# Performance work log

Measured on AMD Instinct MI355X. Metric: run time of the kernel, lower is better.

## Reference

```python
import jax, jax.numpy as jnp
import numpy as np

NUM_NODES = 10000


def setup_inputs() -> dict:
    key = jax.random.key(0)
    k1, k2, k3, k4 = jax.random.split(key, 4)
    x = jax.random.normal(k1, (NUM_NODES, 128), dtype=jnp.float32)
    edge_index = jax.random.randint(k2, (2, 640000), 0, NUM_NODES, dtype=jnp.int64)
    W = jax.random.normal(k3, (128, 128), dtype=jnp.float32) * (1.0 / np.sqrt(128))
    b = jax.random.normal(k4, (128,), dtype=jnp.float32) * 0.01
    return {"x": x, "edge_index": edge_index, "W": W, "b": b}


def reference(x, edge_index, W, b):
    src, dst = edge_index[0], edge_index[1]
    num_nodes = x.shape[0]
    # scatter-add: aggregated[dst] += x[src]
    aggregated = jax.ops.segment_sum(x[src], dst, num_segments=num_nodes)
    # in-degree normalization (clamped at 1)
    degree = jax.ops.segment_sum(jnp.ones_like(dst, dtype=x.dtype), dst,
                                 num_segments=num_nodes)
    degree = jnp.maximum(degree, 1.0)
    aggregated = aggregated / degree[:, None]
    # linear (y = h @ W.T + b) + ReLU
    out = jax.nn.relu(jnp.einsum('nd,od->no', aggregated + x, W) + b)
    return out
```

## Files before the change

### kernel.cpp

```cpp
#include <hip/hip_runtime.h>
#include <hip/hip_bf16.h>
#include <hip/hip_fp8.h>

#define NB    64
#define EPB   10000
#define NPAD  10240
#define NPT   40
#define NGEMM 625
#define LCAP  1024

typedef __bf16 bf16_8 __attribute__((ext_vector_type(8)));
typedef float f32_2 __attribute__((ext_vector_type(2)));
typedef float f32_4 __attribute__((ext_vector_type(4)));
typedef float f32_8 __attribute__((ext_vector_type(8)));

__global__ void __launch_bounds__(256) k_fused(
    const float* __restrict__ x, const float* __restrict__ W,
    const int* __restrict__ ei, int E,
    __hip_bfloat16* __restrict__ zb, unsigned char* __restrict__ zb8,
    unsigned short* __restrict__ bins, unsigned int* __restrict__ combo) {
  __shared__ int h[NPAD / 2];
  __shared__ unsigned short sorted[EPB];
  __shared__ int wsum[4];

  if (blockIdx.x < NGEMM) {
    int rowbase = blockIdx.x * 16;
    int wid = threadIdx.x >> 6;
    int lane = threadIdx.x & 63;
    int m16 = lane & 15;
    int quad = lane >> 4;

    union { bf16_8 v; __hip_bfloat16 h8[8]; } ac[4];
    const float* arow = x + (size_t)(rowbase + m16) * 128 + quad * 8;
#pragma unroll
    for (int kk = 0; kk < 4; ++kk) {
      f32_8 af = *(const f32_8*)(arow + kk * 32);
#pragma unroll
      for (int j = 0; j < 8; ++j) ac[kk].h8[j] = __float2bfloat16(af[j]);
    }
#pragma unroll
    for (int ct = 0; ct < 2; ++ct) {
      int colbase = wid * 32 + ct * 16;
      const float* brow = W + (size_t)(colbase + m16) * 128 + quad * 8;
      f32_4 c = {0.f, 0.f, 0.f, 0.f};
#pragma unroll
      for (int kk = 0; kk < 4; ++kk) {
        f32_8 bf = *(const f32_8*)(brow + kk * 32);
        union { bf16_8 v; __hip_bfloat16 h8[8]; } bc;
#pragma unroll
        for (int j = 0; j < 8; ++j) bc.h8[j] = __float2bfloat16(bf[j]);
        c = __builtin_amdgcn_mfma_f32_16x16x32_bf16(ac[kk].v, bc.v, c, 0, 0, 0);
      }
#pragma unroll
      for (int r = 0; r < 4; ++r) {
        int row = rowbase + quad * 4 + r;
        zb[(size_t)row * 128 + colbase + m16] = __float2bfloat16(c[r]);
        zb8[(size_t)row * 128 + colbase + m16] = __hip_fp8_e4m3(c[r]).__x;
      }
    }
    return;
  }

  const int b = blockIdx.x - NGEMM;
  const int t = threadIdx.x;
  const int4* src4 = (const int4*)(ei) + b * (EPB / 4);
  const int4* dst4 = (const int4*)(ei + E) + b * (EPB / 4);

  for (int i = t; i < NPAD / 2; i += 256) h[i] = 0;
  __syncthreads();

  for (int i = t; i < EPB / 4; i += 256) {
    int4 d = dst4[i];
    atomicAdd(&h[d.x >> 1], 1 << ((d.x & 1) * 16));
    atomicAdd(&h[d.y >> 1], 1 << ((d.y & 1) * 16));
    atomicAdd(&h[d.z >> 1], 1 << ((d.z & 1) * 16));
    atomicAdd(&h[d.w >> 1], 1 << ((d.w & 1) * 16));
  }
  __syncthreads();

  int raw[NPT];
  const int lo = t * NPT;
  int sum = 0;
#pragma unroll
  for (int j = 0; j < NPT; j += 2) {
    int pair = h[(lo + j) >> 1];
    raw[j] = pair & 0xFFFF;
    raw[j + 1] = (pair >> 16) & 0xFFFF;
    sum += raw[j] + raw[j + 1];
  }
  int incl = sum;
#pragma unroll
  for (int off = 1; off < 64; off <<= 1) {
    int v = __shfl_up(incl, off);
    if ((t & 63) >= off) incl += v;
  }
  if ((t & 63) == 63) wsum[t >> 6] = incl;
  __syncthreads();
  int wb = 0;
  for (int w = 0; w < (t >> 6); ++w) wb += wsum[w];
  int run = wb + incl - sum;

  unsigned int cpack[NPT];
#pragma unroll
  for (int j = 0; j < NPT; j += 2) {
    int r0 = run; run += raw[j];
    int r1 = run; run += raw[j + 1];
    h[(lo + j) >> 1] = (r1 << 16) | r0;
    cpack[j]     = ((unsigned)raw[j] << 16) | (unsigned)r0;
    cpack[j + 1] = ((unsigned)raw[j + 1] << 16) | (unsigned)r1;
  }
  __syncthreads();

  unsigned int* crow = combo + (size_t)b * NPAD + lo;
#pragma unroll
  for (int j = 0; j < NPT; j += 4)
    *(uint4*)(crow + j) = make_uint4(cpack[j], cpack[j+1], cpack[j+2], cpack[j+3]);

  for (int i = t; i < EPB / 4; i += 256) {
    int4 s4 = src4[i];
    int4 d4 = dst4[i];
    int ss[4] = {s4.x, s4.y, s4.z, s4.w};
    int dd[4] = {d4.x, d4.y, d4.z, d4.w};
#pragma unroll
    for (int u = 0; u < 4; ++u) {
      int n = dd[u];
      int sh = (n & 1) * 16;
      int pos = (atomicAdd(&h[n >> 1], 1 << sh) >> sh) & 0xFFFF;
      sorted[pos] = (unsigned short)ss[u];
    }
  }
  __syncthreads();

  unsigned int* outb = (unsigned int*)(bins + (size_t)b * EPB);
  const unsigned int* s32 = (const unsigned int*)sorted;
  for (int i = t; i < EPB / 2; i += 256) outb[i] = s32[i];
}

__global__ void __launch_bounds__(256) k_agg(
    const unsigned int* __restrict__ combo, const unsigned short* __restrict__ bins,
    const unsigned char* __restrict__ zb8, const __hip_bfloat16* __restrict__ zb,
    const float* __restrict__ bias, float* __restrict__ out, int N) {
  __shared__ unsigned int trans[4][64];
  __shared__ unsigned short list[4][LCAP];
  __shared__ int cursor[4];

  const int t = threadIdx.x;
  const int wid = t >> 6;
  const int lane = t & 63;
  const int n0 = blockIdx.x * 4;

  if (t < 4) cursor[t] = 0;
  if (t < 64) {
    uint4 cm = *(const uint4*)(combo + (size_t)t * NPAD + n0);
    trans[0][t] = cm.x; trans[1][t] = cm.y; trans[2][t] = cm.z; trans[3][t] = cm.w;
  }
  __syncthreads();

  const int n = n0 + wid;
  unsigned int cc = trans[wid][lane];
  int c = (int)(cc >> 16);
  int o = (int)(cc & 0xFFFF);

  int p = atomicAdd(&cursor[wid], c);

  {
    const unsigned short* bk = bins + (size_t)lane * EPB + o;
    unsigned short s0 = 0, s1 = 0, s2 = 0;
    if (c > 0) s0 = bk[0];
    if (c > 1) s1 = bk[1];
    if (c > 2) s2 = bk[2];
    if (c > 0 && p < LCAP) list[wid][p] = s0;
    if (c > 1 && p + 1 < LCAP) list[wid][p + 1] = s1;
    if (c > 2 && p + 2 < LCAP) list[wid][p + 2] = s2;
    for (int j = 3; j < c; ++j)
      if (p + j < LCAP) list[wid][p + j] = bk[j];
  }
  __syncthreads();

  const int m = cursor[wid];
  const int g = lane >> 4;
  const int sub = lane & 15;
  int mm = m < LCAP ? m : LCAP;

  const unsigned char* z8base = zb8 + sub * 8;

  float acc[8] = {0.f, 0.f, 0.f, 0.f, 0.f, 0.f, 0.f, 0.f};
  for (int e = 0; e < mm; e += 32) {
    uint2 v[8];
#pragma unroll
    for (int u = 0; u < 8; ++u) {
      int idx = e + u * 4 + g;
      v[u] = make_uint2(0u, 0u);
      if (idx < mm) {
        int s = list[wid][idx];
        v[u] = *(const uint2*)(z8base + (size_t)s * 128);
      }
    }
#pragma unroll
    for (int u = 0; u < 8; ++u) {
      f32_2 p01 = __builtin_amdgcn_cvt_pk_f32_fp8((int)v[u].x, false);
      f32_2 p23 = __builtin_amdgcn_cvt_pk_f32_fp8((int)v[u].x, true);
      f32_2 p45 = __builtin_amdgcn_cvt_pk_f32_fp8((int)v[u].y, false);
      f32_2 p67 = __builtin_amdgcn_cvt_pk_f32_fp8((int)v[u].y, true);
      acc[0] += p01[0]; acc[1] += p01[1];
      acc[2] += p23[0]; acc[3] += p23[1];
      acc[4] += p45[0]; acc[5] += p45[1];
      acc[6] += p67[0]; acc[7] += p67[1];
    }
  }
#pragma unroll
  for (int k = 0; k < 8; ++k) {
    acc[k] += __shfl_xor(acc[k], 16);
    acc[k] += __shfl_xor(acc[k], 32);
  }

  if (g == 0 && n < N) {
    float inv = 1.f / (float)(m > 0 ? m : 1);
    bf16_8 zn = *(const bf16_8*)(zb + (size_t)n * 128 + sub * 8);
    f32_8 bv = *(const f32_8*)(bias + sub * 8);
    float r[8];
#pragma unroll
    for (int k = 0; k < 8; ++k) {
      float v2 = acc[k] * inv + (float)zn[k] + bv[k];
      r[k] = v2 > 0.f ? v2 : 0.f;
    }
    float* o2 = out + (size_t)n * 128 + sub * 8;
    *(float4*)(o2)     = make_float4(r[0], r[1], r[2], r[3]);
    *(float4*)(o2 + 4) = make_float4(r[4], r[5], r[6], r[7]);
  }
}

extern "C" void kernel_launch(void* const* d_in, const int* in_sizes, int n_in,
                              void* d_out, int out_size, void* d_ws, size_t ws_size,
                              hipStream_t stream) {
  const float* x = (const float*)d_in[0];
  const int* ei = (const int*)d_in[1];
  const float* W = (const float*)d_in[2];
  const float* b = (const float*)d_in[3];
  float* out = (float*)d_out;

  const int N = in_sizes[0] / 128;
  const int E = in_sizes[1] / 2;

  char* ws = (char*)d_ws;
  size_t off = 0;
  auto carve = [&](size_t bytes) {
    void* p = ws + off;
    off = (off + bytes + 255) & ~(size_t)255;
    return p;
  };
  __hip_bfloat16* zb = (__hip_bfloat16*)carve((size_t)N * 128 * 2);
  unsigned char* zb8 = (unsigned char*)carve((size_t)N * 128);
  unsigned short* bins = (unsigned short*)carve((size_t)NB * EPB * 2);
  unsigned int* combo = (unsigned int*)carve((size_t)NB * NPAD * 4);

  k_fused<<<NGEMM + NB, 256, 0, stream>>>(x, W, ei, E, zb, zb8, bins, combo);
  k_agg<<<N / 4, 256, 0, stream>>>(combo, bins, zb8, zb, b, out, N);
}
```

Measured before the change: 96.46 us.

## Merge GEMM/sort and aggregation into one cooperative kernel with grid sync

Joins the two kernels into a single cooperative launch that separates the GEMM/sort phase from the aggregation phase with a grid-wide barrier, then loops over node quads with a persistent grid. It also stages GEMM outputs through shared memory so the bf16/fp8 stores are coalesced and vectorised, and widens the aggregation gathers to 16-byte loads covering 8 edges per wave step. If the cooperative launch fails or the stream is being captured, it falls back to a two-kernel path. The aim is to remove launch gaps and cut scattered narrow stores, at the cost of grid-sync overhead and fewer resident blocks during aggregation.

Measured after the change: 101.0 us. 1.05x slower.

```diff
diff --git a/kernel.cpp b/kernel.cpp
--- a/kernel.cpp
+++ b/kernel.cpp
@@ -1,6 +1,9 @@
 #include <hip/hip_runtime.h>
 #include <hip/hip_bf16.h>
 #include <hip/hip_fp8.h>
+#include <hip/hip_cooperative_groups.h>
+
+namespace cg = cooperative_groups;
 
 #define NB    64
 #define EPB   10000
@@ -8,60 +11,76 @@
 #define NPT   40
 #define NGEMM 625
 #define LCAP  1024
+#define GRID_FUSED (NGEMM + NB)
+#define SMEM_BYTES 40496
 
 typedef __bf16 bf16_8 __attribute__((ext_vector_type(8)));
 typedef float f32_2 __attribute__((ext_vector_type(2)));
 typedef float f32_4 __attribute__((ext_vector_type(4)));
 typedef float f32_8 __attribute__((ext_vector_type(8)));
 
-__global__ void __launch_bounds__(256) k_fused(
+__device__ __forceinline__ void gemm_role(unsigned char* smem, int bx,
     const float* __restrict__ x, const float* __restrict__ W,
+    __hip_bfloat16* __restrict__ zb, unsigned char* __restrict__ zb8) {
+  float* ctile = (float*)smem;
+  const int rowbase = bx * 16;
+  const int wid = threadIdx.x >> 6;
+  const int lane = threadIdx.x & 63;
+  const int m16 = lane & 15;
+  const int quad = lane >> 4;
+
+  union { bf16_8 v; __hip_bfloat16 h8[8]; } ac[4];
+  const float* arow = x + (size_t)(rowbase + m16) * 128 + quad * 8;
+#pragma unroll
+  for (int kk = 0; kk < 4; ++kk) {
+    f32_8 af = *(const f32_8*)(arow + kk * 32);
+#pragma unroll
+    for (int j = 0; j < 8; ++j) ac[kk].h8[j] = __float2bfloat16(af[j]);
+  }
+#pragma unroll
+  for (int ct = 0; ct < 2; ++ct) {
+    int colbase = wid * 32 + ct * 16;
+    const float* brow = W + (size_t)(colbase + m16) * 128 + quad * 8;
+    f32_4 c = {0.f, 0.f, 0.f, 0.f};
+#pragma unroll
+    for (int kk = 0; kk < 4; ++kk) {
+      f32_8 bf = *(const f32_8*)(brow + kk * 32);
+      union { bf16_8 v; __hip_bfloat16 h8[8]; } bc;
+#pragma unroll
+      for (int j = 0; j < 8; ++j) bc.h8[j] = __float2bfloat16(bf[j]);
+      c = __builtin_amdgcn_mfma_f32_16x16x32_bf16(ac[kk].v, bc.v, c, 0, 0, 0);
+    }
+#pragma unroll
+    for (int r = 0; r < 4; ++r)
+      ctile[(quad * 4 + r) * 132 + colbase + m16] = c[r];
+  }
+  __syncthreads();
+
+  const int row = threadIdx.x >> 4;
+  const int cs = (threadIdx.x & 15) * 8;
+  const float* src = ctile + row * 132 + cs;
+  f32_4 a0 = *(const f32_4*)(src);
+  f32_4 a1 = *(const f32_4*)(src + 4);
+  union { uint4 u; __hip_bfloat16 h[8]; } hb;
+  union { uint2 u; unsigned char c[8]; } q8;
+#pragma unroll
+  for (int j = 0; j < 4; ++j) {
+    hb.h[j] = __float2bfloat16(a0[j]);
+    hb.h[4 + j] = __float2bfloat16(a1[j]);
+    q8.c[j] = __hip_fp8_e4m3(a0[j]).__x;
+    q8.c[4 + j] = __hip_fp8_e4m3(a1[j]).__x;
+  }
+  *(uint4*)(zb + (size_t)(rowbase + row) * 128 + cs) = hb.u;
+  *(uint2*)(zb8 + (size_t)(rowbase + row) * 128 + cs) = q8.u;
+}
+
+__device__ __forceinline__ void sort_role(unsigned char* smem, int b,
     const int* __restrict__ ei, int E,
-    __hip_bfloat16* __restrict__ zb, unsigned char* __restrict__ zb8,
     unsigned short* __restrict__ bins, unsigned int* __restrict__ combo) {
-  __shared__ int h[NPAD / 2];
-  __shared__ unsigned short sorted[EPB];
-  __shared__ int wsum[4];
-
-  if (blockIdx.x < NGEMM) {
-    int rowbase = blockIdx.x * 16;
-    int wid = threadIdx.x >> 6;
-    int lane = threadIdx.x & 63;
-    int m16 = lane & 15;
-    int quad = lane >> 4;
-
-    union { bf16_8 v; __hip_bfloat16 h8[8]; } ac[4];
-    const float* arow = x + (size_t)(rowbase + m16) * 128 + quad * 8;
-#pragma unroll
-    for (int kk = 0; kk < 4; ++kk) {
-      f32_8 af = *(const f32_8*)(arow + kk * 32);
-#pragma unroll
-      for (int j = 0; j < 8; ++j) ac[kk].h8[j] = __float2bfloat16(af[j]);
-    }
-#pragma unroll
-    for (int ct = 0; ct < 2; ++ct) {
-      int colbase = wid * 32 + ct * 16;
-      const float* brow = W + (size_t)(colbase + m16) * 128 + quad * 8;
-      f32_4 c = {0.f, 0.f, 0.f, 0.f};
-#pragma unroll
-      for (int kk = 0; kk < 4; ++kk) {
-        f32_8 bf = *(const f32_8*)(brow + kk * 32);
-        union { bf16_8 v; __hip_bfloat16 h8[8]; } bc;
-#pragma unroll
-        for (int j = 0; j < 8; ++j) bc.h8[j] = __float2bfloat16(bf[j]);
-        c = __builtin_amdgcn_mfma_f32_16x16x32_bf16(ac[kk].v, bc.v, c, 0, 0, 0);
-      }
-#pragma unroll
-      for (int r = 0; r < 4; ++r) {
-        int row = rowbase + quad * 4 + r;
-        zb[(size_t)row * 128 + colbase + m16] = __float2bfloat16(c[r]);
-        zb8[(size_t)row * 128 + colbase + m16] = __hip_fp8_e4m3(c[r]).__x;
-      }
-    }
-    return;
-  }
-
-  const int b = blockIdx.x - NGEMM;
+  int* h = (int*)smem;
+  unsigned short* sorted = (unsigned short*)(smem + 20480);
+  int* wsum = (int*)(smem + 40480);
+
   const int t = threadIdx.x;
   const int4* src4 = (const int4*)(ei) + b * (EPB / 4);
   const int4* dst4 = (const int4*)(ei + E) + b * (EPB / 4);
@@ -123,9 +142,9 @@
     int dd[4] = {d4.x, d4.y, d4.z, d4.w};
 #pragma unroll
     for (int u = 0; u < 4; ++u) {
-      int n = dd[u];
-      int sh = (n & 1) * 16;
-      int pos = (atomicAdd(&h[n >> 1], 1 << sh) >> sh) & 0xFFFF;
+      int nn = dd[u];
+      int sh = (nn & 1) * 16;
+      int pos = (atomicAdd(&h[nn >> 1], 1 << sh) >> sh) & 0xFFFF;
       sorted[pos] = (unsigned short)ss[u];
     }
   }
@@ -136,28 +155,29 @@
   for (int i = t; i < EPB / 2; i += 256) outb[i] = s32[i];
 }
 
-__global__ void __launch_bounds__(256) k_agg(
+__device__ __forceinline__ void agg_quad(unsigned char* smem, int q,
     const unsigned int* __restrict__ combo, const unsigned short* __restrict__ bins,
     const unsigned char* __restrict__ zb8, const __hip_bfloat16* __restrict__ zb,
     const float* __restrict__ bias, float* __restrict__ out, int N) {
-  __shared__ unsigned int trans[4][64];
-  __shared__ unsigned short list[4][LCAP];
-  __shared__ int cursor[4];
+  unsigned int* trans = (unsigned int*)smem;
+  unsigned short* list = (unsigned short*)(smem + 1024);
+  int* cursor = (int*)(smem + 9216);
 
   const int t = threadIdx.x;
   const int wid = t >> 6;
   const int lane = t & 63;
-  const int n0 = blockIdx.x * 4;
-
+  const int n0 = q * 4;
+
+  __syncthreads();
   if (t < 4) cursor[t] = 0;
   if (t < 64) {
     uint4 cm = *(const uint4*)(combo + (size_t)t * NPAD + n0);
-    trans[0][t] = cm.x; trans[1][t] = cm.y; trans[2][t] = cm.z; trans[3][t] = cm.w;
+    trans[t] = cm.x; trans[64 + t] = cm.y; trans[128 + t] = cm.z; trans[192 + t] = cm.w;
   }
   __syncthreads();
 
   const int n = n0 + wid;
-  unsigned int cc = trans[wid][lane];
+  unsigned int cc = trans[wid * 64 + lane];
   int c = (int)(cc >> 16);
   int o = (int)(cc & 0xFFFF);
 
@@ -165,35 +185,39 @@
 
   {
     const unsigned short* bk = bins + (size_t)lane * EPB + o;
+    unsigned short* L = list + wid * LCAP;
     unsigned short s0 = 0, s1 = 0, s2 = 0;
     if (c > 0) s0 = bk[0];
     if (c > 1) s1 = bk[1];
     if (c > 2) s2 = bk[2];
-    if (c > 0 && p < LCAP) list[wid][p] = s0;
-    if (c > 1 && p + 1 < LCAP) list[wid][p + 1] = s1;
-    if (c > 2 && p + 2 < LCAP) list[wid][p + 2] = s2;
+    if (c > 0 && p < LCAP) L[p] = s0;
+    if (c > 1 && p + 1 < LCAP) L[p + 1] = s1;
+    if (c > 2 && p + 2 < LCAP) L[p + 2] = s2;
     for (int j = 3; j < c; ++j)
-      if (p + j < LCAP) list[wid][p + j] = bk[j];
+      if (p + j < LCAP) L[p + j] = bk[j];
   }
   __syncthreads();
 
   const int m = cursor[wid];
-  const int g = lane >> 4;
-  const int sub = lane & 15;
+  const int g = lane >> 3;
+  const int sub = lane & 7;
   int mm = m < LCAP ? m : LCAP;
-
-  const unsigned char* z8base = zb8 + sub * 8;
-
-  float acc[8] = {0.f, 0.f, 0.f, 0.f, 0.f, 0.f, 0.f, 0.f};
-  for (int e = 0; e < mm; e += 32) {
-    uint2 v[8];
+  const unsigned short* L = list + wid * LCAP;
+  const unsigned char* z8base = zb8 + sub * 16;
+
+  float acc[16];
+#pragma unroll
+  for (int k = 0; k < 16; ++k) acc[k] = 0.f;
+
+  for (int e = 0; e < mm; e += 64) {
+    uint4 v[8];
 #pragma unroll
     for (int u = 0; u < 8; ++u) {
-      int idx = e + u * 4 + g;
-      v[u] = make_uint2(0u, 0u);
+      int idx = e + u * 8 + g;
+      v[u] = make_uint4(0u, 0u, 0u, 0u);
       if (idx < mm) {
-        int s = list[wid][idx];
-        v[u] = *(const uint2*)(z8base + (size_t)s * 128);
+        int s = L[idx];
+        v[u] = *(const uint4*)(z8base + (size_t)s * 128);
       }
     }
 #pragma unroll
@@ -202,32 +226,82 @@
       f32_2 p23 = __builtin_amdgcn_cvt_pk_f32_fp8((int)v[u].x, true);
       f32_2 p45 = __builtin_amdgcn_cvt_pk_f32_fp8((int)v[u].y, false);
       f32_2 p67 = __builtin_amdgcn_cvt_pk_f32_fp8((int)v[u].y, true);
-      acc[0] += p01[0]; acc[1] += p01[1];
-      acc[2] += p23[0]; acc[3] += p23[1];
-      acc[4] += p45[0]; acc[5] += p45[1];
-      acc[6] += p67[0]; acc[7] += p67[1];
-    }
-  }
-#pragma unroll
-  for (int k = 0; k < 8; ++k) {
+      f32_2 p89 = __builtin_amdgcn_cvt_pk_f32_fp8((int)v[u].z, false);
+      f32_2 pab = __builtin_amdgcn_cvt_pk_f32_fp8((int)v[u].z, true);
+      f32_2 pcd = __builtin_amdgcn_cvt_pk_f32_fp8((int)v[u].w, false);
+      f32_2 pef = __builtin_amdgcn_cvt_pk_f32_fp8((int)v[u].w, true);
+      acc[0] += p01[0];  acc[1] += p01[1];  acc[2] += p23[0];  acc[3] += p23[1];
+      acc[4] += p45[0];  acc[5] += p45[1];  acc[6] += p67[0];  acc[7] += p67[1];
+      acc[8] += p89[0];  acc[9] += p89[1];  acc[10] += pab[0]; acc[11] += pab[1];
+      acc[12] += pcd[0]; acc[13] += pcd[1]; acc[14] += pef[0]; acc[15] += pef[1];
+    }
+  }
+#pragma unroll
+  for (int k = 0; k < 16; ++k) {
+    acc[k] += __shfl_xor(acc[k], 8);
     acc[k] += __shfl_xor(acc[k], 16);
     acc[k] += __shfl_xor(acc[k], 32);
   }
 
   if (g == 0 && n < N) {
     float inv = 1.f / (float)(m > 0 ? m : 1);
-    bf16_8 zn = *(const bf16_8*)(zb + (size_t)n * 128 + sub * 8);
-    f32_8 bv = *(const f32_8*)(bias + sub * 8);
-    float r[8];
+    const __hip_bfloat16* znp = zb + (size_t)n * 128 + sub * 16;
+    bf16_8 z0 = *(const bf16_8*)znp;
+    bf16_8 z1 = *(const bf16_8*)(znp + 8);
+    const float* bp = bias + sub * 16;
+    f32_8 b0 = *(const f32_8*)bp;
+    f32_8 b1 = *(const f32_8*)(bp + 8);
+    float r[16];
 #pragma unroll
     for (int k = 0; k < 8; ++k) {
-      float v2 = acc[k] * inv + (float)zn[k] + bv[k];
+      float v2 = acc[k] * inv + (float)z0[k] + b0[k];
       r[k] = v2 > 0.f ? v2 : 0.f;
     }
-    float* o2 = out + (size_t)n * 128 + sub * 8;
-    *(float4*)(o2)     = make_float4(r[0], r[1], r[2], r[3]);
-    *(float4*)(o2 + 4) = make_float4(r[4], r[5], r[6], r[7]);
-  }
+#pragma unroll
+    for (int k = 0; k < 8; ++k) {
+      float v2 = acc[8 + k] * inv + (float)z1[k] + b1[k];
+      r[8 + k] = v2 > 0.f ? v2 : 0.f;
+    }
+    float* o2 = out + (size_t)n * 128 + sub * 16;
+    *(float4*)(o2)      = make_float4(r[0], r[1], r[2], r[3]);
+    *(float4*)(o2 + 4)  = make_float4(r[4], r[5], r[6], r[7]);
+    *(float4*)(o2 + 8)  = make_float4(r[8], r[9], r[10], r[11]);
+    *(float4*)(o2 + 12) = make_float4(r[12], r[13], r[14], r[15]);
+  }
+}
+
+__global__ void __launch_bounds__(256, 3) k_all(
+    const float* __restrict__ x, const int* __restrict__ ei,
+    const float* __restrict__ W, const float* __restrict__ bias,
+    __hip_bfloat16* __restrict__ zb, unsigned char* __restrict__ zb8,
+    unsigned short* __restrict__ bins, unsigned int* __restrict__ combo,
+    float* __restrict__ out, int E, int N) {
+  __shared__ __align__(16) unsigned char smem[SMEM_BYTES];
+  if (blockIdx.x < NGEMM) gemm_role(smem, blockIdx.x, x, W, zb, zb8);
+  else sort_role(smem, blockIdx.x - NGEMM, ei, E, bins, combo);
+  __threadfence();
+  cg::this_grid().sync();
+  const int NQ = N >> 2;
+  for (int q = blockIdx.x; q < NQ; q += gridDim.x)
+    agg_quad(smem, q, combo, bins, zb8, zb, bias, out, N);
+}
+
+__global__ void __launch_bounds__(256, 3) k_phase1(
+    const float* __restrict__ x, const int* __restrict__ ei,
+    const float* __restrict__ W,
+    __hip_bfloat16* __restrict__ zb, unsigned char* __restrict__ zb8,
+    unsigned short* __restrict__ bins, unsigned int* __restrict__ combo, int E) {
+  __shared__ __align__(16) unsigned char smem[SMEM_BYTES];
+  if (blockIdx.x < NGEMM) gemm_role(smem, blockIdx.x, x, W, zb, zb8);
+  else sort_role(smem, blockIdx.x - NGEMM, ei, E, bins, combo);
+}
+
+__global__ void __launch_bounds__(256) k_phase2(
+    const unsigned int* __restrict__ combo, const unsigned short* __restrict__ bins,
+    const unsigned char* __restrict__ zb8, const __hip_bfloat16* __restrict__ zb,
+    const float* __restrict__ bias, float* __restrict__ out, int N) {
+  __shared__ __align__(16) unsigned char smem[9232];
+  agg_quad(smem, blockIdx.x, combo, bins, zb8, zb, bias, out, N);
 }
 
 extern "C" void kernel_launch(void* const* d_in, const int* in_sizes, int n_in,
@@ -254,6 +328,32 @@
   unsigned short* bins = (unsigned short*)carve((size_t)NB * EPB * 2);
   unsigned int* combo = (unsigned int*)carve((size_t)NB * NPAD * 4);
 
-  k_fused<<<NGEMM + NB, 256, 0, stream>>>(x, W, ei, E, zb, zb8, bins, combo);
-  k_agg<<<N / 4, 256, 0, stream>>>(combo, bins, zb8, zb, b, out, N);
-}
+  static int coop = -1;
+  bool done = false;
+  if (coop != 0) {
+    bool try_now = true;
+    if (coop == -1) {
+      hipStreamCaptureStatus st = hipStreamCaptureStatusNone;
+      (void)hipStreamIsCapturing(stream, &st);
+      if (st != hipStreamCaptureStatusNone) try_now = false;
+    }
+    if (try_now) {
+      void* args[] = {(void*)&x, (void*)&ei, (void*)&W, (void*)&b,
+                      (void*)&zb, (void*)&zb8, (void*)&bins, (void*)&combo,
+                      (void*)&out, (void*)&E, (void*)&N};
+      hipError_t err = hipLaunchCooperativeKernel((const void*)k_all, dim3(GRID_FUSED),
+                                                  dim3(256), args, 0, stream);
+      if (err == hipSuccess) {
+        coop = 1;
+        done = true;
+      } else {
+        coop = 0;
+        (void)hipGetLastError();
+      }
+    }
+  }
+  if (!done) {
+    k_phase1<<<GRID_FUSED, 256, 0, stream>>>(x, ei, W, zb, zb8, bins, combo, E);
+    k_phase2<<<N / 4, 256, 0, stream>>>(combo, bins, zb8, zb, b, out, N);
+  }
+}
```

## Split edge sort into 256 bins, inline first two sources, stage GEMM output in LDS

Applied to the files above, without the earlier changes.

Edge binning now uses 256 blocks of 2500 edges instead of 64 blocks of 10000. The per-node combo record grows to 8 bytes and carries the first two sorted source ids, so the aggregation kernel rarely has to read the bins array. Aggregation replaces the LDS atomic cursor with a wave prefix scan over four bins per lane, and sort blocks now launch before GEMM blocks. The GEMM output is staged through shared memory so bf16/fp8 stores are vectorised, in exchange for a larger combo array that each aggregation block reads in full (256 entries per node group).

After: 108.7 us. 12.7% more time.

```diff
diff --git a/kernel.cpp b/kernel.cpp
--- a/kernel.cpp
+++ b/kernel.cpp
@@ -2,66 +2,81 @@
 #include <hip/hip_bf16.h>
 #include <hip/hip_fp8.h>
 
-#define NB    64
-#define EPB   10000
+#define NB    256
+#define EPB   2500
 #define NPAD  10240
 #define NPT   40
 #define NGEMM 625
 #define LCAP  1024
+#define SMEM_BYTES 25496
 
 typedef __bf16 bf16_8 __attribute__((ext_vector_type(8)));
 typedef float f32_2 __attribute__((ext_vector_type(2)));
 typedef float f32_4 __attribute__((ext_vector_type(4)));
 typedef float f32_8 __attribute__((ext_vector_type(8)));
 
-__global__ void __launch_bounds__(256) k_fused(
+__device__ __forceinline__ void gemm_role(unsigned char* smem, int bx,
     const float* __restrict__ x, const float* __restrict__ W,
+    __hip_bfloat16* __restrict__ zb, unsigned char* __restrict__ zb8) {
+  float* ctile = (float*)smem;
+  const int rowbase = bx * 16;
+  const int wid = threadIdx.x >> 6;
+  const int lane = threadIdx.x & 63;
+  const int m16 = lane & 15;
+  const int quad = lane >> 4;
+
+  union { bf16_8 v; __hip_bfloat16 h8[8]; } ac[4];
+  const float* arow = x + (size_t)(rowbase + m16) * 128 + quad * 8;
+#pragma unroll
+  for (int kk = 0; kk < 4; ++kk) {
+    f32_8 af = *(const f32_8*)(arow + kk * 32);
+#pragma unroll
+    for (int j = 0; j < 8; ++j) ac[kk].h8[j] = __float2bfloat16(af[j]);
+  }
+#pragma unroll
+  for (int ct = 0; ct < 2; ++ct) {
+    int colbase = wid * 32 + ct * 16;
+    const float* brow = W + (size_t)(colbase + m16) * 128 + quad * 8;
+    f32_4 c = {0.f, 0.f, 0.f, 0.f};
+#pragma unroll
+    for (int kk = 0; kk < 4; ++kk) {
+      f32_8 bf = *(const f32_8*)(brow + kk * 32);
+      union { bf16_8 v; __hip_bfloat16 h8[8]; } bc;
+#pragma unroll
+      for (int j = 0; j < 8; ++j) bc.h8[j] = __float2bfloat16(bf[j]);
+      c = __builtin_amdgcn_mfma_f32_16x16x32_bf16(ac[kk].v, bc.v, c, 0, 0, 0);
+    }
+#pragma unroll
+    for (int r = 0; r < 4; ++r)
+      ctile[(quad * 4 + r) * 132 + colbase + m16] = c[r];
+  }
+  __syncthreads();
+
+  const int row = threadIdx.x >> 4;
+  const int cs = (threadIdx.x & 15) * 8;
+  const float* src = ctile + row * 132 + cs;
+  f32_4 a0 = *(const f32_4*)(src);
+  f32_4 a1 = *(const f32_4*)(src + 4);
+  union { uint4 u; __hip_bfloat16 h[8]; } hb;
+  union { uint2 u; unsigned char c[8]; } q8;
+#pragma unroll
+  for (int j = 0; j < 4; ++j) {
+    hb.h[j] = __float2bfloat16(a0[j]);
+    hb.h[4 + j] = __float2bfloat16(a1[j]);
+    q8.c[j] = __hip_fp8_e4m3(a0[j]).__x;
+    q8.c[4 + j] = __hip_fp8_e4m3(a1[j]).__x;
+  }
+  *(uint4*)(zb + (size_t)(rowbase + row) * 128 + cs) = hb.u;
+  *(uint2*)(zb8 + (size_t)(rowbase + row) * 128 + cs) = q8.u;
+}
+
+__device__ __forceinline__ void sort_role(unsigned char* smem, int b,
     const int* __restrict__ ei, int E,
-    __hip_bfloat16* __restrict__ zb, unsigned char* __restrict__ zb8,
-    unsigned short* __restrict__ bins, unsigned int* __restrict__ combo) {
-  __shared__ int h[NPAD / 2];
-  __shared__ unsigned short sorted[EPB];
-  __shared__ int wsum[4];
-
-  if (blockIdx.x < NGEMM) {
-    int rowbase = blockIdx.x * 16;
-    int wid = threadIdx.x >> 6;
-    int lane = threadIdx.x & 63;
-    int m16 = lane & 15;
-    int quad = lane >> 4;
-
-    union { bf16_8 v; __hip_bfloat16 h8[8]; } ac[4];
-    const float* arow = x + (size_t)(rowbase + m16) * 128 + quad * 8;
-#pragma unroll
-    for (int kk = 0; kk < 4; ++kk) {
-      f32_8 af = *(const f32_8*)(arow + kk * 32);
-#pragma unroll
-      for (int j = 0; j < 8; ++j) ac[kk].h8[j] = __float2bfloat16(af[j]);
-    }
-#pragma unroll
-    for (int ct = 0; ct < 2; ++ct) {
-      int colbase = wid * 32 + ct * 16;
-      const float* brow = W + (size_t)(colbase + m16) * 128 + quad * 8;
-      f32_4 c = {0.f, 0.f, 0.f, 0.f};
-#pragma unroll
-      for (int kk = 0; kk < 4; ++kk) {
-        f32_8 bf = *(const f32_8*)(brow + kk * 32);
-        union { bf16_8 v; __hip_bfloat16 h8[8]; } bc;
-#pragma unroll
-        for (int j = 0; j < 8; ++j) bc.h8[j] = __float2bfloat16(bf[j]);
-        c = __builtin_amdgcn_mfma_f32_16x16x32_bf16(ac[kk].v, bc.v, c, 0, 0, 0);
-      }
-#pragma unroll
-      for (int r = 0; r < 4; ++r) {
-        int row = rowbase + quad * 4 + r;
-        zb[(size_t)row * 128 + colbase + m16] = __float2bfloat16(c[r]);
-        zb8[(size_t)row * 128 + colbase + m16] = __hip_fp8_e4m3(c[r]).__x;
-      }
-    }
-    return;
-  }
-
-  const int b = blockIdx.x - NGEMM;
+    unsigned short* __restrict__ bins, uint2* __restrict__ combo) {
+  int* h = (int*)smem;
+  unsigned short* sorted = (unsigned short*)(smem + 20480);
+  int* wsum = (int*)(smem + 25480);
+
   const int t = threadIdx.x;
   const int4* src4 = (const int4*)(ei) + b * (EPB / 4);
   const int4* dst4 = (const int4*)(ei + E) + b * (EPB / 4);
@@ -111,11 +126,6 @@
   }
   __syncthreads();
 
-  unsigned int* crow = combo + (size_t)b * NPAD + lo;
-#pragma unroll
-  for (int j = 0; j < NPT; j += 4)
-    *(uint4*)(crow + j) = make_uint4(cpack[j], cpack[j+1], cpack[j+2], cpack[j+3]);
-
   for (int i = t; i < EPB / 4; i += 256) {
     int4 s4 = src4[i];
     int4 d4 = dst4[i];
@@ -123,65 +133,103 @@
     int dd[4] = {d4.x, d4.y, d4.z, d4.w};
 #pragma unroll
     for (int u = 0; u < 4; ++u) {
-      int n = dd[u];
-      int sh = (n & 1) * 16;
-      int pos = (atomicAdd(&h[n >> 1], 1 << sh) >> sh) & 0xFFFF;
+      int nn = dd[u];
+      int sh = (nn & 1) * 16;
+      int pos = (atomicAdd(&h[nn >> 1], 1 << sh) >> sh) & 0xFFFF;
       sorted[pos] = (unsigned short)ss[u];
     }
   }
   __syncthreads();
+
+  uint2* crow = combo + (size_t)b * NPAD + lo;
+#pragma unroll
+  for (int j = 0; j < NPT; ++j) {
+    unsigned int hi = cpack[j];
+    int c = (int)(hi >> 16);
+    int o = (int)(hi & 0xFFFF);
+    unsigned int s0 = (c > 0) ? (unsigned int)sorted[o] : 0u;
+    unsigned int s1 = (c > 1) ? (unsigned int)sorted[o + 1] : 0u;
+    crow[j] = make_uint2(s0 | (s1 << 16), hi);
+  }
 
   unsigned int* outb = (unsigned int*)(bins + (size_t)b * EPB);
   const unsigned int* s32 = (const unsigned int*)sorted;
   for (int i = t; i < EPB / 2; i += 256) outb[i] = s32[i];
 }
 
+__global__ void __launch_bounds__(256) k_phase1(
+    const float* __restrict__ x, const int* __restrict__ ei,
+    const float* __restrict__ W,
+    __hip_bfloat16* __restrict__ zb, unsigned char* __restrict__ zb8,
+    unsigned short* __restrict__ bins, uint2* __restrict__ combo, int E) {
+  __shared__ __align__(16) unsigned char smem[SMEM_BYTES];
+  if (blockIdx.x < NB) sort_role(smem, blockIdx.x, ei, E, bins, combo);
+  else gemm_role(smem, blockIdx.x - NB, x, W, zb, zb8);
+}
+
 __global__ void __launch_bounds__(256) k_agg(
-    const unsigned int* __restrict__ combo, const unsigned short* __restrict__ bins,
+    const uint2* __restrict__ combo, const unsigned short* __restrict__ bins,
     const unsigned char* __restrict__ zb8, const __hip_bfloat16* __restrict__ zb,
     const float* __restrict__ bias, float* __restrict__ out, int N) {
-  __shared__ unsigned int trans[4][64];
+  __shared__ uint2 tr[4][256];
   __shared__ unsigned short list[4][LCAP];
-  __shared__ int cursor[4];
 
   const int t = threadIdx.x;
   const int wid = t >> 6;
   const int lane = t & 63;
   const int n0 = blockIdx.x * 4;
 
-  if (t < 4) cursor[t] = 0;
-  if (t < 64) {
-    uint4 cm = *(const uint4*)(combo + (size_t)t * NPAD + n0);
-    trans[0][t] = cm.x; trans[1][t] = cm.y; trans[2][t] = cm.z; trans[3][t] = cm.w;
+  {
+    const uint4* p = (const uint4*)(combo + (size_t)t * NPAD + n0);
+    uint4 a = p[0];
+    uint4 bq = p[1];
+    tr[0][t] = make_uint2(a.x, a.y);
+    tr[1][t] = make_uint2(a.z, a.w);
+    tr[2][t] = make_uint2(bq.x, bq.y);
+    tr[3][t] = make_uint2(bq.z, bq.w);
   }
   __syncthreads();
 
   const int n = n0 + wid;
-  unsigned int cc = trans[wid][lane];
-  int c = (int)(cc >> 16);
-  int o = (int)(cc & 0xFFFF);
-
-  int p = atomicAdd(&cursor[wid], c);
-
-  {
-    const unsigned short* bk = bins + (size_t)lane * EPB + o;
-    unsigned short s0 = 0, s1 = 0, s2 = 0;
-    if (c > 0) s0 = bk[0];
-    if (c > 1) s1 = bk[1];
-    if (c > 2) s2 = bk[2];
-    if (c > 0 && p < LCAP) list[wid][p] = s0;
-    if (c > 1 && p + 1 < LCAP) list[wid][p + 1] = s1;
-    if (c > 2 && p + 2 < LCAP) list[wid][p + 2] = s2;
-    for (int j = 3; j < c; ++j)
-      if (p + j < LCAP) list[wid][p + j] = bk[j];
-  }
-  __syncthreads();
-
-  const int m = cursor[wid];
+  uint2 e0 = tr[wid][lane];
+  uint2 e1 = tr[wid][lane + 64];
+  uint2 e2 = tr[wid][lane + 128];
+  uint2 e3 = tr[wid][lane + 192];
+  const int c0 = (int)(e0.y >> 16), c1 = (int)(e1.y >> 16);
+  const int c2 = (int)(e2.y >> 16), c3 = (int)(e3.y >> 16);
+  const int ctot = c0 + c1 + c2 + c3;
+
+  int incl = ctot;
+#pragma unroll
+  for (int off = 1; off < 64; off <<= 1) {
+    int v = __shfl_up(incl, off);
+    if (lane >= off) incl += v;
+  }
+  const int m = __shfl(incl, 63);
+  int off = incl - ctot;
+
+  unsigned short* L = list[wid];
+#define SEG(E, C, K)                                                          \
+  do {                                                                        \
+    if ((C) > 0 && off < LCAP) L[off] = (unsigned short)((E).x & 0xFFFF);     \
+    if ((C) > 1 && off + 1 < LCAP) L[off + 1] = (unsigned short)((E).x >> 16);\
+    if ((C) > 2) {                                                            \
+      const unsigned short* bk =                                              \
+          bins + (size_t)(lane + 64 * (K)) * EPB + ((E).y & 0xFFFF);          \
+      for (int j = 2; j < (C); ++j)                                           \
+        if (off + j < LCAP) L[off + j] = bk[j];                               \
+    }                                                                         \
+    off += (C);                                                               \
+  } while (0)
+  SEG(e0, c0, 0);
+  SEG(e1, c1, 1);
+  SEG(e2, c2, 2);
+  SEG(e3, c3, 3);
+#undef SEG
+
   const int g = lane >> 4;
   const int sub = lane & 15;
   int mm = m < LCAP ? m : LCAP;
-
   const unsigned char* z8base = zb8 + sub * 8;
 
   float acc[8] = {0.f, 0.f, 0.f, 0.f, 0.f, 0.f, 0.f, 0.f};
@@ -192,7 +240,7 @@
       int idx = e + u * 4 + g;
       v[u] = make_uint2(0u, 0u);
       if (idx < mm) {
-        int s = list[wid][idx];
+        int s = L[idx];
         v[u] = *(const uint2*)(z8base + (size_t)s * 128);
       }
     }
@@ -252,8 +300,8 @@
   __hip_bfloat16* zb = (__hip_bfloat16*)carve((size_t)N * 128 * 2);
   unsigned char* zb8 = (unsigned char*)carve((size_t)N * 128);
   unsigned short* bins = (unsigned short*)carve((size_t)NB * EPB * 2);
-  unsigned int* combo = (unsigned int*)carve((size_t)NB * NPAD * 4);
-
-  k_fused<<<NGEMM + NB, 256, 0, stream>>>(x, W, ei, E, zb, zb8, bins, combo);
+  uint2* combo = (uint2*)carve((size_t)NB * NPAD * 8);
+
+  k_phase1<<<NB + NGEMM, 256, 0, stream>>>(x, ei, W, zb, zb8, bins, combo, E);
   k_agg<<<N / 4, 256, 0, stream>>>(combo, bins, zb8, zb, b, out, N);
 }
```
